# Optimization experiments

Measured on AMD Instinct MI355X. Metric: run time of the kernel, lower is better.

Reference implementation:

```python
import jax, jax.numpy as jnp
import numpy as np

N_USERS = 50000
N_ITEMS = 150000
N = N_USERS + N_ITEMS
N_EDGES = 1250000
D = 64
N_LAYERS = 3


def setup_inputs() -> dict:
    key = jax.random.key(0)
    ks = jax.random.split(key, 7)
    edge_src = jax.random.randint(ks[0], (N_EDGES,), 0, N, dtype=jnp.int32)
    edge_dst = jax.random.randint(ks[1], (N_EDGES,), 0, N, dtype=jnp.int32)
    edge_weight = jax.random.uniform(ks[2], (N_EDGES,), dtype=jnp.float32)
    user_emb = jax.random.normal(ks[3], (N_USERS, D), dtype=jnp.float32) * 0.1
    item_emb = jax.random.normal(ks[4], (N_ITEMS, D), dtype=jnp.float32) * 0.1
    # Ws[layer, which_linear] with which_linear in {0: W1 (on L@e), 1: W2 (on (L@e)*e), 2: W3 (on e)}
    Ws = jax.random.normal(ks[5], (N_LAYERS, 3, D, D), dtype=jnp.float32) * (1.0 / np.sqrt(D))
    bs = jnp.zeros((N_LAYERS, 3, D), dtype=jnp.float32)
    return {"edge_src": edge_src, "edge_dst": edge_dst, "edge_weight": edge_weight,
            "user_emb": user_emb, "item_emb": item_emb, "Ws": Ws, "bs": bs}


def _l2_normalize(x):
    # torch.nn.functional.normalize(p=2, dim=1, eps=1e-12)
    n = jnp.sqrt(jnp.sum(x * x, axis=1, keepdims=True))
    return x / jnp.maximum(n, 1e-12)


def reference(edge_src, edge_dst, edge_weight, user_emb, item_emb, Ws, bs):
    e = jnp.concatenate([user_emb, item_emb], axis=0)  # [N, D]
    all_embs = [e]
    for i in range(N_LAYERS):
        # SpMM: term1 = L @ e (COO scatter-add)
        term1 = jax.ops.segment_sum(edge_weight[:, None] * e[edge_src], edge_dst,
                                    num_segments=N)  # [N, D]
        term2 = term1 * e
        inter = (term1 @ Ws[i, 0] + bs[i, 0]
                 + term2 @ Ws[i, 1] + bs[i, 1]
                 + e @ Ws[i, 2] + bs[i, 2])
        inter = jax.nn.leaky_relu(inter, negative_slope=0.01)
        e = _l2_normalize(inter)  # dropout is identity in eval mode
        all_embs.append(e)
    all_embs = jnp.concatenate(all_embs, axis=1)  # [N, 4*D]
    return all_embs[:N_USERS], all_embs[N_USERS:]
```

## Files before the change

kernel.cpp:

```cpp
#include <hip/hip_runtime.h>
#include <hip/hip_bf16.h>

#define NU 50000
#define NI 150000
#define NN 200000
#define NE 1250000
#define DD 64
#define NLAYERS 3
#define SCAN_B 1024
#define NB ((NN + SCAN_B - 1) / SCAN_B)
#define BT_STRIDE 232

typedef __attribute__((ext_vector_type(8))) short bf16x8;
typedef __attribute__((ext_vector_type(4))) float f32x4;

static __device__ __forceinline__ unsigned short f2b(float x) {
  __hip_bfloat16 h = __float2bfloat16(x);
  return *reinterpret_cast<unsigned short*>(&h);
}

static __device__ __forceinline__ unsigned int pack2(float lo, float hi) {
  return (unsigned int)f2b(lo) | ((unsigned int)f2b(hi) << 16);
}

static __device__ __forceinline__ float blo(unsigned int u) { return __uint_as_float(u << 16); }
static __device__ __forceinline__ float bhi(unsigned int u) { return __uint_as_float(u & 0xffff0000u); }

static __device__ __forceinline__ bf16x8 mulbf8(bf16x8 a, bf16x8 b) {
  union { bf16x8 v; unsigned int u[4]; } A, B, R;
  A.v = a; B.v = b;
#pragma unroll
  for (int i = 0; i < 4; ++i) {
    R.u[i] = pack2(blo(A.u[i]) * blo(B.u[i]), bhi(A.u[i]) * bhi(B.u[i]));
  }
  return R.v;
}

__global__ __launch_bounds__(256) void k_setup(const float4* __restrict__ ue,
                                               const float4* __restrict__ ie,
                                               float4* __restrict__ out4,
                                               uint2* __restrict__ ebf2,
                                               const float* __restrict__ Ws,
                                               unsigned short* __restrict__ WtBf,
                                               int* __restrict__ cnt) {
  int gid = blockIdx.x * 256 + threadIdx.x;
  if (gid < NN * 16) {
    int row = gid >> 4, q = gid & 15;
    float4 v = (row < NU) ? ue[(size_t)row * 16 + q] : ie[(size_t)(row - NU) * 16 + q];
    out4[(size_t)row * 64 + q] = v;
    uint2 b; b.x = pack2(v.x, v.y); b.y = pack2(v.z, v.w);
    ebf2[(size_t)row * 16 + q] = b;
  }
  if (gid < NN) cnt[gid] = 0;
  if (gid < 3 * 64 * 192) {
    int j = gid % 192;
    int n = (gid / 192) & 63;
    int lyr = gid / (192 * 64);
    WtBf[gid] = f2b(Ws[((size_t)lyr * 3 + (j >> 6)) * 4096 + (size_t)(j & 63) * 64 + n]);
  }
}

__global__ __launch_bounds__(256) void k_hist(const int* __restrict__ dst, int* __restrict__ cnt) {
  int e = blockIdx.x * 256 + threadIdx.x;
  if (e < NE) atomicAdd(&cnt[dst[e]], 1);
}

__global__ __launch_bounds__(SCAN_B) void k_scan1(const int* __restrict__ cnt,
                                                  int* __restrict__ local,
                                                  int* __restrict__ btot) {
  __shared__ int sm[SCAN_B];
  int t = threadIdx.x;
  int i = blockIdx.x * SCAN_B + t;
  int v = (i < NN) ? cnt[i] : 0;
  sm[t] = v;
  __syncthreads();
  for (int off = 1; off < SCAN_B; off <<= 1) {
    int x = (t >= off) ? sm[t - off] : 0;
    __syncthreads();
    sm[t] += x;
    __syncthreads();
  }
  if (i < NN) local[i] = sm[t] - v;
  if (t == SCAN_B - 1) btot[blockIdx.x] = sm[t];
}

__global__ __launch_bounds__(256) void k_scan2(int* __restrict__ btot) {
  __shared__ int sm[256];
  int t = threadIdx.x;
  int v = (t < NB) ? btot[t] : 0;
  sm[t] = v;
  __syncthreads();
  for (int off = 1; off < 256; off <<= 1) {
    int x = (t >= off) ? sm[t - off] : 0;
    __syncthreads();
    sm[t] += x;
    __syncthreads();
  }
  if (t < NB) btot[t] = sm[t] - v;
}

__global__ __launch_bounds__(256) void k_finalize(const int* __restrict__ local,
                                                  const int* __restrict__ btot,
                                                  int* __restrict__ row_start,
                                                  int* __restrict__ cursor) {
  int i = blockIdx.x * 256 + threadIdx.x;
  if (i < NN) {
    int v = local[i] + btot[i / SCAN_B];
    row_start[i] = v;
    cursor[i] = v;
  }
  if (i == 0) row_start[NN] = NE;
}

__global__ __launch_bounds__(256) void k_fill(const int* __restrict__ src,
                                              const int* __restrict__ dst,
                                              const float* __restrict__ w,
                                              int* __restrict__ cursor,
                                              int2* __restrict__ csr_pack) {
  int e = blockIdx.x * 256 + threadIdx.x;
  if (e < NE) {
    int p = atomicAdd(&cursor[dst[e]], 1);
    int2 pk; pk.x = src[e]; pk.y = __float_as_int(w[e]);
    csr_pack[p] = pk;
  }
}

__global__ __launch_bounds__(256) void k_spmm(const int* __restrict__ row_start,
                                              const int2* __restrict__ csr_pack,
                                              const unsigned int* __restrict__ ebf,
                                              unsigned int* __restrict__ t1bf) {
  int gid = blockIdx.x * 256 + threadIdx.x;
  int row = gid >> 6;
  if (row >= NN) return;
  const int l = gid & 63;
  const int eidx = l >> 3;
  const int cb = l & 7;
  int s0 = row_start[row];
  int s1 = row_start[row + 1];
  int deg = s1 - s0;

  float a0 = 0.f, a1 = 0.f, a2 = 0.f, a3 = 0.f, a4 = 0.f, a5 = 0.f, a6 = 0.f, a7 = 0.f;

  if (deg > 0) {
    int j0 = s0 + eidx;
    bool e0 = j0 < s1;
    j0 = e0 ? j0 : s1 - 1;
    int2 p0 = csr_pack[j0];
    uint4 v0 = *reinterpret_cast<const uint4*>(ebf + (size_t)p0.x * 32 + cb * 4);
    float w0 = e0 ? __int_as_float(p0.y) : 0.f;
    if (deg > 8) {
      int j1 = s0 + 8 + eidx;
      bool e1 = j1 < s1;
      j1 = e1 ? j1 : s1 - 1;
      int2 p1 = csr_pack[j1];
      uint4 v1 = *reinterpret_cast<const uint4*>(ebf + (size_t)p1.x * 32 + cb * 4);
      float w1 = e1 ? __int_as_float(p1.y) : 0.f;
      a0 = fmaf(w0, blo(v0.x), a0); a1 = fmaf(w0, bhi(v0.x), a1);
      a2 = fmaf(w0, blo(v0.y), a2); a3 = fmaf(w0, bhi(v0.y), a3);
      a4 = fmaf(w0, blo(v0.z), a4); a5 = fmaf(w0, bhi(v0.z), a5);
      a6 = fmaf(w0, blo(v0.w), a6); a7 = fmaf(w0, bhi(v0.w), a7);
      a0 = fmaf(w1, blo(v1.x), a0); a1 = fmaf(w1, bhi(v1.x), a1);
      a2 = fmaf(w1, blo(v1.y), a2); a3 = fmaf(w1, bhi(v1.y), a3);
      a4 = fmaf(w1, blo(v1.z), a4); a5 = fmaf(w1, bhi(v1.z), a5);
      a6 = fmaf(w1, blo(v1.w), a6); a7 = fmaf(w1, bhi(v1.w), a7);
      for (int base = s0 + 16; base < s1; base += 8) {
        int j = base + eidx;
        bool ev = j < s1;
        j = ev ? j : s1 - 1;
        int2 p = csr_pack[j];
        uint4 v = *reinterpret_cast<const uint4*>(ebf + (size_t)p.x * 32 + cb * 4);
        float wt = ev ? __int_as_float(p.y) : 0.f;
        a0 = fmaf(wt, blo(v.x), a0); a1 = fmaf(wt, bhi(v.x), a1);
        a2 = fmaf(wt, blo(v.y), a2); a3 = fmaf(wt, bhi(v.y), a3);
        a4 = fmaf(wt, blo(v.z), a4); a5 = fmaf(wt, bhi(v.z), a5);
        a6 = fmaf(wt, blo(v.w), a6); a7 = fmaf(wt, bhi(v.w), a7);
      }
    } else {
      a0 = fmaf(w0, blo(v0.x), a0); a1 = fmaf(w0, bhi(v0.x), a1);
      a2 = fmaf(w0, blo(v0.y), a2); a3 = fmaf(w0, bhi(v0.y), a3);
      a4 = fmaf(w0, blo(v0.z), a4); a5 = fmaf(w0, bhi(v0.z), a5);
      a6 = fmaf(w0, blo(v0.w), a6); a7 = fmaf(w0, bhi(v0.w), a7);
    }
  }

  a0 += __shfl_xor(a0, 8, 64);  a0 += __shfl_xor(a0, 16, 64);  a0 += __shfl_xor(a0, 32, 64);
  a1 += __shfl_xor(a1, 8, 64);  a1 += __shfl_xor(a1, 16, 64);  a1 += __shfl_xor(a1, 32, 64);
  a2 += __shfl_xor(a2, 8, 64);  a2 += __shfl_xor(a2, 16, 64);  a2 += __shfl_xor(a2, 32, 64);
  a3 += __shfl_xor(a3, 8, 64);  a3 += __shfl_xor(a3, 16, 64);  a3 += __shfl_xor(a3, 32, 64);
  a4 += __shfl_xor(a4, 8, 64);  a4 += __shfl_xor(a4, 16, 64);  a4 += __shfl_xor(a4, 32, 64);
  a5 += __shfl_xor(a5, 8, 64);  a5 += __shfl_xor(a5, 16, 64);  a5 += __shfl_xor(a5, 32, 64);
  a6 += __shfl_xor(a6, 8, 64);  a6 += __shfl_xor(a6, 16, 64);  a6 += __shfl_xor(a6, 32, 64);
  a7 += __shfl_xor(a7, 8, 64);  a7 += __shfl_xor(a7, 16, 64);  a7 += __shfl_xor(a7, 32, 64);

  if (l < 8) {
    uint4 st;
    st.x = pack2(a0, a1); st.y = pack2(a2, a3); st.z = pack2(a4, a5); st.w = pack2(a6, a7);
    *reinterpret_cast<uint4*>(t1bf + (size_t)row * 32 + l * 4) = st;
  }
}

__global__ __launch_bounds__(512) void k_row_mfma(const unsigned int* __restrict__ t1bf,
                                                  const unsigned int* __restrict__ ebf,
                                                  const unsigned short* __restrict__ WtBf,
                                                  const float* __restrict__ bs,
                                                  float* __restrict__ out,
                                                  unsigned short* __restrict__ ebf_next,
                                                  int layer, int wbf) {
  __shared__ unsigned short Bt[64][BT_STRIDE];
  const int tid = threadIdx.x;
  {
    const uint4* __restrict__ src = reinterpret_cast<const uint4*>(WtBf + (size_t)layer * 64 * 192);
#pragma unroll
    for (int ch = tid; ch < 1536; ch += 512) {
      int rown = ch / 24, k = ch % 24;
      *reinterpret_cast<uint4*>(&Bt[rown][k * 8]) = src[ch];
    }
  }
  __syncthreads();

  const int l = tid & 63;
  const int wv = tid >> 6;
  const int g = l >> 4;
  const int li = l & 15;
  const int rowbase = blockIdx.x * 128 + wv * 16;
  if (rowbase >= NN) return;
  const int r = rowbase + li;

  const unsigned short* __restrict__ t1b = reinterpret_cast<const unsigned short*>(t1bf);
  const unsigned short* __restrict__ eb = reinterpret_cast<const unsigned short*>(ebf);
  bf16x8 A0 = *reinterpret_cast<const bf16x8*>(t1b + (size_t)r * 64 + 8 * g);
  bf16x8 A1 = *reinterpret_cast<const bf16x8*>(t1b + (size_t)r * 64 + 32 + 8 * g);
  bf16x8 E0 = *reinterpret_cast<const bf16x8*>(eb + (size_t)r * 64 + 8 * g);
  bf16x8 E1 = *reinterpret_cast<const bf16x8*>(eb + (size_t)r * 64 + 32 + 8 * g);
  bf16x8 T0 = mulbf8(A0, E0);
  bf16x8 T1 = mulbf8(A1, E1);

  const float* __restrict__ bsl = bs + (size_t)layer * 3 * 64;
  f32x4 acc[4];
#pragma unroll
  for (int f = 0; f < 4; ++f) {
    int n = f * 16 + li;
    float bv = bsl[n] + bsl[64 + n] + bsl[128 + n];
    acc[f] = (f32x4){bv, bv, bv, bv};
  }

  bf16x8 Afr[6] = {A0, A1, T0, T1, E0, E1};
#pragma unroll
  for (int s = 0; s < 6; ++s) {
#pragma unroll
    for (int f = 0; f < 4; ++f) {
      const bf16x8 Bf = *reinterpret_cast<const bf16x8*>(&Bt[f * 16 + li][s * 32 + 8 * g]);
      acc[f] = __builtin_amdgcn_mfma_f32_16x16x32_bf16(Afr[s], Bf, acc[f], 0, 0, 0);
    }
  }

  float p[4];
#pragma unroll
  for (int reg = 0; reg < 4; ++reg) {
    float ssum = 0.f;
#pragma unroll
    for (int f = 0; f < 4; ++f) {
      float x = acc[f][reg];
      x = (x >= 0.f) ? x : 0.01f * x;
      acc[f][reg] = x;
      ssum = fmaf(x, x, ssum);
    }
    p[reg] = ssum;
  }
#pragma unroll
  for (int off = 1; off < 16; off <<= 1) {
#pragma unroll
    for (int reg = 0; reg < 4; ++reg) p[reg] += __shfl_xor(p[reg], off, 64);
  }
  float inv[4];
#pragma unroll
  for (int reg = 0; reg < 4; ++reg) inv[reg] = 1.0f / fmaxf(sqrtf(p[reg]), 1e-12f);

  float* __restrict__ ob = out + (size_t)(layer + 1) * 64;
#pragma unroll
  for (int reg = 0; reg < 4; ++reg) {
#pragma unroll
    for (int f = 0; f < 4; ++f) {
      float val = acc[f][reg] * inv[reg];
      ob[(size_t)(rowbase + 4 * g + reg) * 256 + f * 16 + li] = val;
      if (wbf) ebf_next[(size_t)(rowbase + 4 * g + reg) * 64 + f * 16 + li] = f2b(val);
    }
  }
}

extern "C" void kernel_launch(void* const* d_in, const int* in_sizes, int n_in,
                              void* d_out, int out_size, void* d_ws, size_t ws_size,
                              hipStream_t stream) {
  const int* edge_src = (const int*)d_in[0];
  const int* edge_dst = (const int*)d_in[1];
  const float* edge_w = (const float*)d_in[2];
  const float* user_emb = (const float*)d_in[3];
  const float* item_emb = (const float*)d_in[4];
  const float* Ws = (const float*)d_in[5];
  const float* bs = (const float*)d_in[6];
  float* out = (float*)d_out;

  char* w = (char*)d_ws;
  unsigned int* ebfA = (unsigned int*)w; w += (size_t)NN * 32 * 4;
  unsigned int* ebfB = (unsigned int*)w; w += (size_t)NN * 32 * 4;
  unsigned int* t1bf = (unsigned int*)w; w += (size_t)NN * 32 * 4;
  int2* csr_pack = (int2*)w;      w += (size_t)NE * 8;
  unsigned short* WtBf = (unsigned short*)w; w += (size_t)3 * 64 * 192 * 2;
  int* cnt = (int*)w;             w += (size_t)NN * 4;
  int* local = (int*)w;           w += (size_t)NN * 4;
  int* row_start = (int*)w;       w += (size_t)(NN + 4) * 4;
  int* cursor = (int*)w;          w += (size_t)NN * 4;
  int* btot = (int*)w;            w += 256 * 4;

  k_setup<<<(NN * 16 + 255) / 256, 256, 0, stream>>>(
      (const float4*)user_emb, (const float4*)item_emb, (float4*)out, (uint2*)ebfA,
      Ws, WtBf, cnt);
  k_hist<<<(NE + 255) / 256, 256, 0, stream>>>(edge_dst, cnt);
  k_scan1<<<NB, SCAN_B, 0, stream>>>(cnt, local, btot);
  k_scan2<<<1, 256, 0, stream>>>(btot);
  k_finalize<<<(NN + 255) / 256, 256, 0, stream>>>(local, btot, row_start, cursor);
  k_fill<<<(NE + 255) / 256, 256, 0, stream>>>(edge_src, edge_dst, edge_w, cursor, csr_pack);

  k_spmm<<<(NN * 64 + 255) / 256, 256, 0, stream>>>(row_start, csr_pack, ebfA, t1bf);
  k_row_mfma<<<(NN + 127) / 128, 512, 0, stream>>>(t1bf, ebfA, WtBf, bs, out, (unsigned short*)ebfB, 0, 1);
  k_spmm<<<(NN * 64 + 255) / 256, 256, 0, stream>>>(row_start, csr_pack, ebfB, t1bf);
  k_row_mfma<<<(NN + 127) / 128, 512, 0, stream>>>(t1bf, ebfB, WtBf, bs, out, (unsigned short*)ebfA, 1, 1);
  k_spmm<<<(NN * 64 + 255) / 256, 256, 0, stream>>>(row_start, csr_pack, ebfA, t1bf);
  k_row_mfma<<<(NN + 127) / 128, 512, 0, stream>>>(t1bf, ebfA, WtBf, bs, out, (unsigned short*)ebfB, 2, 0);
}
```

Baseline: 412.6 us.

## Fuse SpMM with per-row MFMA transform into one layer kernel; merge setup with histogram

Each layer now runs as one kernel. Sixteen waves each gather one row's neighbours into shared memory, then four waves run the MFMA transform on those 16 rows, each wave handling a 16-column slice, with the L2 norm reduced across waves through shared memory. This drops the t1 round trip through global memory and one launch per layer. The cost is that every 1024-thread block loads the full 24 KB weight tile for only 16 rows, and 12 of the 16 waves sit idle during the MFMA phase. Separately, the setup and histogram kernels are merged into one launch, with a small kernel added in front to zero the counters.

```diff
diff --git a/kernel.cpp b/kernel.cpp
--- a/kernel.cpp
+++ b/kernel.cpp
@@ -10,6 +10,8 @@
 #define SCAN_B 1024
 #define NB ((NN + SCAN_B - 1) / SCAN_B)
 #define BT_STRIDE 232
+#define SETUP_BLKS 12500
+#define HIST_BLKS ((NE + 255) / 256)
 
 typedef __attribute__((ext_vector_type(8))) short bf16x8;
 typedef __attribute__((ext_vector_type(4))) float f32x4;
@@ -36,33 +38,37 @@
   return R.v;
 }
 
-__global__ __launch_bounds__(256) void k_setup(const float4* __restrict__ ue,
-                                               const float4* __restrict__ ie,
-                                               float4* __restrict__ out4,
-                                               uint2* __restrict__ ebf2,
-                                               const float* __restrict__ Ws,
-                                               unsigned short* __restrict__ WtBf,
-                                               int* __restrict__ cnt) {
-  int gid = blockIdx.x * 256 + threadIdx.x;
-  if (gid < NN * 16) {
+__global__ __launch_bounds__(256) void k_zero(int* __restrict__ p) {
+  int i = blockIdx.x * 256 + threadIdx.x;
+  if (i < NN) p[i] = 0;
+}
+
+__global__ __launch_bounds__(256) void k_setup_hist(const float4* __restrict__ ue,
+                                                    const float4* __restrict__ ie,
+                                                    float4* __restrict__ out4,
+                                                    uint2* __restrict__ ebf2,
+                                                    const float* __restrict__ Ws,
+                                                    unsigned short* __restrict__ WtBf,
+                                                    const int* __restrict__ dst,
+                                                    int* __restrict__ cnt) {
+  int bid = blockIdx.x;
+  if (bid < SETUP_BLKS) {
+    int gid = bid * 256 + threadIdx.x;
     int row = gid >> 4, q = gid & 15;
     float4 v = (row < NU) ? ue[(size_t)row * 16 + q] : ie[(size_t)(row - NU) * 16 + q];
     out4[(size_t)row * 64 + q] = v;
     uint2 b; b.x = pack2(v.x, v.y); b.y = pack2(v.z, v.w);
     ebf2[(size_t)row * 16 + q] = b;
-  }
-  if (gid < NN) cnt[gid] = 0;
-  if (gid < 3 * 64 * 192) {
-    int j = gid % 192;
-    int n = (gid / 192) & 63;
-    int lyr = gid / (192 * 64);
-    WtBf[gid] = f2b(Ws[((size_t)lyr * 3 + (j >> 6)) * 4096 + (size_t)(j & 63) * 64 + n]);
-  }
-}
-
-__global__ __launch_bounds__(256) void k_hist(const int* __restrict__ dst, int* __restrict__ cnt) {
-  int e = blockIdx.x * 256 + threadIdx.x;
-  if (e < NE) atomicAdd(&cnt[dst[e]], 1);
+    if (gid < 3 * 64 * 192) {
+      int j = gid % 192;
+      int n = (gid / 192) & 63;
+      int lyr = gid / (192 * 64);
+      WtBf[gid] = f2b(Ws[((size_t)lyr * 3 + (j >> 6)) * 4096 + (size_t)(j & 63) * 64 + n]);
+    }
+  } else {
+    int e = (bid - SETUP_BLKS) * 256 + threadIdx.x;
+    if (e < NE) atomicAdd(&cnt[dst[e]], 1);
+  }
 }
 
 __global__ __launch_bounds__(SCAN_B) void k_scan1(const int* __restrict__ cnt,
@@ -125,165 +131,155 @@
   }
 }
 
-__global__ __launch_bounds__(256) void k_spmm(const int* __restrict__ row_start,
-                                              const int2* __restrict__ csr_pack,
-                                              const unsigned int* __restrict__ ebf,
-                                              unsigned int* __restrict__ t1bf) {
-  int gid = blockIdx.x * 256 + threadIdx.x;
-  int row = gid >> 6;
-  if (row >= NN) return;
-  const int l = gid & 63;
-  const int eidx = l >> 3;
-  const int cb = l & 7;
-  int s0 = row_start[row];
-  int s1 = row_start[row + 1];
-  int deg = s1 - s0;
-
-  float a0 = 0.f, a1 = 0.f, a2 = 0.f, a3 = 0.f, a4 = 0.f, a5 = 0.f, a6 = 0.f, a7 = 0.f;
-
-  if (deg > 0) {
-    int j0 = s0 + eidx;
-    bool e0 = j0 < s1;
-    j0 = e0 ? j0 : s1 - 1;
-    int2 p0 = csr_pack[j0];
-    uint4 v0 = *reinterpret_cast<const uint4*>(ebf + (size_t)p0.x * 32 + cb * 4);
-    float w0 = e0 ? __int_as_float(p0.y) : 0.f;
-    if (deg > 8) {
-      int j1 = s0 + 8 + eidx;
-      bool e1 = j1 < s1;
-      j1 = e1 ? j1 : s1 - 1;
-      int2 p1 = csr_pack[j1];
-      uint4 v1 = *reinterpret_cast<const uint4*>(ebf + (size_t)p1.x * 32 + cb * 4);
-      float w1 = e1 ? __int_as_float(p1.y) : 0.f;
-      a0 = fmaf(w0, blo(v0.x), a0); a1 = fmaf(w0, bhi(v0.x), a1);
-      a2 = fmaf(w0, blo(v0.y), a2); a3 = fmaf(w0, bhi(v0.y), a3);
-      a4 = fmaf(w0, blo(v0.z), a4); a5 = fmaf(w0, bhi(v0.z), a5);
-      a6 = fmaf(w0, blo(v0.w), a6); a7 = fmaf(w0, bhi(v0.w), a7);
-      a0 = fmaf(w1, blo(v1.x), a0); a1 = fmaf(w1, bhi(v1.x), a1);
-      a2 = fmaf(w1, blo(v1.y), a2); a3 = fmaf(w1, bhi(v1.y), a3);
-      a4 = fmaf(w1, blo(v1.z), a4); a5 = fmaf(w1, bhi(v1.z), a5);
-      a6 = fmaf(w1, blo(v1.w), a6); a7 = fmaf(w1, bhi(v1.w), a7);
-      for (int base = s0 + 16; base < s1; base += 8) {
-        int j = base + eidx;
-        bool ev = j < s1;
-        j = ev ? j : s1 - 1;
-        int2 p = csr_pack[j];
-        uint4 v = *reinterpret_cast<const uint4*>(ebf + (size_t)p.x * 32 + cb * 4);
-        float wt = ev ? __int_as_float(p.y) : 0.f;
-        a0 = fmaf(wt, blo(v.x), a0); a1 = fmaf(wt, bhi(v.x), a1);
-        a2 = fmaf(wt, blo(v.y), a2); a3 = fmaf(wt, bhi(v.y), a3);
-        a4 = fmaf(wt, blo(v.z), a4); a5 = fmaf(wt, bhi(v.z), a5);
-        a6 = fmaf(wt, blo(v.w), a6); a7 = fmaf(wt, bhi(v.w), a7);
-      }
-    } else {
-      a0 = fmaf(w0, blo(v0.x), a0); a1 = fmaf(w0, bhi(v0.x), a1);
-      a2 = fmaf(w0, blo(v0.y), a2); a3 = fmaf(w0, bhi(v0.y), a3);
-      a4 = fmaf(w0, blo(v0.z), a4); a5 = fmaf(w0, bhi(v0.z), a5);
-      a6 = fmaf(w0, blo(v0.w), a6); a7 = fmaf(w0, bhi(v0.w), a7);
-    }
-  }
-
-  a0 += __shfl_xor(a0, 8, 64);  a0 += __shfl_xor(a0, 16, 64);  a0 += __shfl_xor(a0, 32, 64);
-  a1 += __shfl_xor(a1, 8, 64);  a1 += __shfl_xor(a1, 16, 64);  a1 += __shfl_xor(a1, 32, 64);
-  a2 += __shfl_xor(a2, 8, 64);  a2 += __shfl_xor(a2, 16, 64);  a2 += __shfl_xor(a2, 32, 64);
-  a3 += __shfl_xor(a3, 8, 64);  a3 += __shfl_xor(a3, 16, 64);  a3 += __shfl_xor(a3, 32, 64);
-  a4 += __shfl_xor(a4, 8, 64);  a4 += __shfl_xor(a4, 16, 64);  a4 += __shfl_xor(a4, 32, 64);
-  a5 += __shfl_xor(a5, 8, 64);  a5 += __shfl_xor(a5, 16, 64);  a5 += __shfl_xor(a5, 32, 64);
-  a6 += __shfl_xor(a6, 8, 64);  a6 += __shfl_xor(a6, 16, 64);  a6 += __shfl_xor(a6, 32, 64);
-  a7 += __shfl_xor(a7, 8, 64);  a7 += __shfl_xor(a7, 16, 64);  a7 += __shfl_xor(a7, 32, 64);
-
-  if (l < 8) {
-    uint4 st;
-    st.x = pack2(a0, a1); st.y = pack2(a2, a3); st.z = pack2(a4, a5); st.w = pack2(a6, a7);
-    *reinterpret_cast<uint4*>(t1bf + (size_t)row * 32 + l * 4) = st;
-  }
-}
-
-__global__ __launch_bounds__(512) void k_row_mfma(const unsigned int* __restrict__ t1bf,
-                                                  const unsigned int* __restrict__ ebf,
-                                                  const unsigned short* __restrict__ WtBf,
-                                                  const float* __restrict__ bs,
-                                                  float* __restrict__ out,
-                                                  unsigned short* __restrict__ ebf_next,
-                                                  int layer, int wbf) {
+__global__ __launch_bounds__(1024, 8) void k_layer(const int* __restrict__ row_start,
+                                                   const int2* __restrict__ csr_pack,
+                                                   const unsigned int* __restrict__ ebf,
+                                                   const unsigned short* __restrict__ WtBf,
+                                                   const float* __restrict__ bs,
+                                                   float* __restrict__ out,
+                                                   unsigned short* __restrict__ ebf_next,
+                                                   int layer, int wbf) {
   __shared__ unsigned short Bt[64][BT_STRIDE];
+  __shared__ unsigned short t1s[16][72];
+  __shared__ float rsum[4][16];
+
   const int tid = threadIdx.x;
+  const int wv = tid >> 6;
+  const int l = tid & 63;
+
   {
     const uint4* __restrict__ src = reinterpret_cast<const uint4*>(WtBf + (size_t)layer * 64 * 192);
-#pragma unroll
-    for (int ch = tid; ch < 1536; ch += 512) {
+    for (int ch = tid; ch < 1536; ch += 1024) {
       int rown = ch / 24, k = ch % 24;
       *reinterpret_cast<uint4*>(&Bt[rown][k * 8]) = src[ch];
     }
   }
+
+  {
+    const int row = blockIdx.x * 16 + wv;
+    const int eidx = l >> 3;
+    const int cb = l & 7;
+    int s0 = row_start[row];
+    int s1 = row_start[row + 1];
+    int deg = s1 - s0;
+
+    float a0 = 0.f, a1 = 0.f, a2 = 0.f, a3 = 0.f, a4 = 0.f, a5 = 0.f, a6 = 0.f, a7 = 0.f;
+
+    if (deg > 0) {
+      int j0 = s0 + eidx;
+      bool e0 = j0 < s1;
+      j0 = e0 ? j0 : s1 - 1;
+      int2 p0 = csr_pack[j0];
+      uint4 v0 = *reinterpret_cast<const uint4*>(ebf + (size_t)p0.x * 32 + cb * 4);
+      float w0 = e0 ? __int_as_float(p0.y) : 0.f;
+      if (deg > 8) {
+        int j1 = s0 + 8 + eidx;
+        bool e1 = j1 < s1;
+        j1 = e1 ? j1 : s1 - 1;
+        int2 p1 = csr_pack[j1];
+        uint4 v1 = *reinterpret_cast<const uint4*>(ebf + (size_t)p1.x * 32 + cb * 4);
+        float w1 = e1 ? __int_as_float(p1.y) : 0.f;
+        a0 = fmaf(w0, blo(v0.x), a0); a1 = fmaf(w0, bhi(v0.x), a1);
+        a2 = fmaf(w0, blo(v0.y), a2); a3 = fmaf(w0, bhi(v0.y), a3);
+        a4 = fmaf(w0, blo(v0.z), a4); a5 = fmaf(w0, bhi(v0.z), a5);
+        a6 = fmaf(w0, blo(v0.w), a6); a7 = fmaf(w0, bhi(v0.w), a7);
+        a0 = fmaf(w1, blo(v1.x), a0); a1 = fmaf(w1, bhi(v1.x), a1);
+        a2 = fmaf(w1, blo(v1.y), a2); a3 = fmaf(w1, bhi(v1.y), a3);
+        a4 = fmaf(w1, blo(v1.z), a4); a5 = fmaf(w1, bhi(v1.z), a5);
+        a6 = fmaf(w1, blo(v1.w), a6); a7 = fmaf(w1, bhi(v1.w), a7);
+        for (int base = s0 + 16; base < s1; base += 8) {
+          int j = base + eidx;
+          bool ev = j < s1;
+          j = ev ? j : s1 - 1;
+          int2 p = csr_pack[j];
+          uint4 v = *reinterpret_cast<const uint4*>(ebf + (size_t)p.x * 32 + cb * 4);
+          float wt = ev ? __int_as_float(p.y) : 0.f;
+          a0 = fmaf(wt, blo(v.x), a0); a1 = fmaf(wt, bhi(v.x), a1);
+          a2 = fmaf(wt, blo(v.y), a2); a3 = fmaf(wt, bhi(v.y), a3);
+          a4 = fmaf(wt, blo(v.z), a4); a5 = fmaf(wt, bhi(v.z), a5);
+          a6 = fmaf(wt, blo(v.w), a6); a7 = fmaf(wt, bhi(v.w), a7);
+        }
+      } else {
+        a0 = fmaf(w0, blo(v0.x), a0); a1 = fmaf(w0, bhi(v0.x), a1);
+        a2 = fmaf(w0, blo(v0.y), a2); a3 = fmaf(w0, bhi(v0.y), a3);
+        a4 = fmaf(w0, blo(v0.z), a4); a5 = fmaf(w0, bhi(v0.z), a5);
+        a6 = fmaf(w0, blo(v0.w), a6); a7 = fmaf(w0, bhi(v0.w), a7);
+      }
+    }
+
+    a0 += __shfl_xor(a0, 8, 64);  a0 += __shfl_xor(a0, 16, 64);  a0 += __shfl_xor(a0, 32, 64);
+    a1 += __shfl_xor(a1, 8, 64);  a1 += __shfl_xor(a1, 16, 64);  a1 += __shfl_xor(a1, 32, 64);
+    a2 += __shfl_xor(a2, 8, 64);  a2 += __shfl_xor(a2, 16, 64);  a2 += __shfl_xor(a2, 32, 64);
+    a3 += __shfl_xor(a3, 8, 64);  a3 += __shfl_xor(a3, 16, 64);  a3 += __shfl_xor(a3, 32, 64);
+    a4 += __shfl_xor(a4, 8, 64);  a4 += __shfl_xor(a4, 16, 64);  a4 += __shfl_xor(a4, 32, 64);
+    a5 += __shfl_xor(a5, 8, 64);  a5 += __shfl_xor(a5, 16, 64);  a5 += __shfl_xor(a5, 32, 64);
+    a6 += __shfl_xor(a6, 8, 64);  a6 += __shfl_xor(a6, 16, 64);  a6 += __shfl_xor(a6, 32, 64);
+    a7 += __shfl_xor(a7, 8, 64);  a7 += __shfl_xor(a7, 16, 64);  a7 += __shfl_xor(a7, 32, 64);
+
+    if (l < 8) {
+      uint4 st;
+      st.x = pack2(a0, a1); st.y = pack2(a2, a3); st.z = pack2(a4, a5); st.w = pack2(a6, a7);
+      *reinterpret_cast<uint4*>(&t1s[wv][l * 8]) = st;
+    }
+  }
   __syncthreads();
 
-  const int l = tid & 63;
-  const int wv = tid >> 6;
   const int g = l >> 4;
   const int li = l & 15;
-  const int rowbase = blockIdx.x * 128 + wv * 16;
-  if (rowbase >= NN) return;
-  const int r = rowbase + li;
-
-  const unsigned short* __restrict__ t1b = reinterpret_cast<const unsigned short*>(t1bf);
-  const unsigned short* __restrict__ eb = reinterpret_cast<const unsigned short*>(ebf);
-  bf16x8 A0 = *reinterpret_cast<const bf16x8*>(t1b + (size_t)r * 64 + 8 * g);
-  bf16x8 A1 = *reinterpret_cast<const bf16x8*>(t1b + (size_t)r * 64 + 32 + 8 * g);
-  bf16x8 E0 = *reinterpret_cast<const bf16x8*>(eb + (size_t)r * 64 + 8 * g);
-  bf16x8 E1 = *reinterpret_cast<const bf16x8*>(eb + (size_t)r * 64 + 32 + 8 * g);
-  bf16x8 T0 = mulbf8(A0, E0);
-  bf16x8 T1 = mulbf8(A1, E1);
-
-  const float* __restrict__ bsl = bs + (size_t)layer * 3 * 64;
-  f32x4 acc[4];
-#pragma unroll
-  for (int f = 0; f < 4; ++f) {
-    int n = f * 16 + li;
+  f32x4 acc = (f32x4){0.f, 0.f, 0.f, 0.f};
+  if (wv < 4) {
+    const int r = blockIdx.x * 16 + li;
+    bf16x8 A0 = *reinterpret_cast<const bf16x8*>(&t1s[li][8 * g]);
+    bf16x8 A1 = *reinterpret_cast<const bf16x8*>(&t1s[li][32 + 8 * g]);
+    const unsigned short* __restrict__ eb = reinterpret_cast<const unsigned short*>(ebf);
+    bf16x8 E0 = *reinterpret_cast<const bf16x8*>(eb + (size_t)r * 64 + 8 * g);
+    bf16x8 E1 = *reinterpret_cast<const bf16x8*>(eb + (size_t)r * 64 + 32 + 8 * g);
+    bf16x8 T0 = mulbf8(A0, E0);
+    bf16x8 T1 = mulbf8(A1, E1);
+
+    const float* __restrict__ bsl = bs + (size_t)layer * 3 * 64;
+    int n = wv * 16 + li;
     float bv = bsl[n] + bsl[64 + n] + bsl[128 + n];
-    acc[f] = (f32x4){bv, bv, bv, bv};
-  }
-
-  bf16x8 Afr[6] = {A0, A1, T0, T1, E0, E1};
-#pragma unroll
-  for (int s = 0; s < 6; ++s) {
-#pragma unroll
-    for (int f = 0; f < 4; ++f) {
-      const bf16x8 Bf = *reinterpret_cast<const bf16x8*>(&Bt[f * 16 + li][s * 32 + 8 * g]);
-      acc[f] = __builtin_amdgcn_mfma_f32_16x16x32_bf16(Afr[s], Bf, acc[f], 0, 0, 0);
-    }
-  }
-
-  float p[4];
-#pragma unroll
-  for (int reg = 0; reg < 4; ++reg) {
-    float ssum = 0.f;
-#pragma unroll
-    for (int f = 0; f < 4; ++f) {
-      float x = acc[f][reg];
+    acc = (f32x4){bv, bv, bv, bv};
+
+    bf16x8 Afr[6] = {A0, A1, T0, T1, E0, E1};
+#pragma unroll
+    for (int s = 0; s < 6; ++s) {
+      const bf16x8 Bf = *reinterpret_cast<const bf16x8*>(&Bt[wv * 16 + li][s * 32 + 8 * g]);
+      acc = __builtin_amdgcn_mfma_f32_16x16x32_bf16(Afr[s], Bf, acc, 0, 0, 0);
+    }
+
+    float p[4];
+#pragma unroll
+    for (int reg = 0; reg < 4; ++reg) {
+      float x = acc[reg];
       x = (x >= 0.f) ? x : 0.01f * x;
-      acc[f][reg] = x;
-      ssum = fmaf(x, x, ssum);
-    }
-    p[reg] = ssum;
-  }
-#pragma unroll
-  for (int off = 1; off < 16; off <<= 1) {
-#pragma unroll
-    for (int reg = 0; reg < 4; ++reg) p[reg] += __shfl_xor(p[reg], off, 64);
-  }
-  float inv[4];
-#pragma unroll
-  for (int reg = 0; reg < 4; ++reg) inv[reg] = 1.0f / fmaxf(sqrtf(p[reg]), 1e-12f);
-
-  float* __restrict__ ob = out + (size_t)(layer + 1) * 64;
-#pragma unroll
-  for (int reg = 0; reg < 4; ++reg) {
-#pragma unroll
-    for (int f = 0; f < 4; ++f) {
-      float val = acc[f][reg] * inv[reg];
-      ob[(size_t)(rowbase + 4 * g + reg) * 256 + f * 16 + li] = val;
-      if (wbf) ebf_next[(size_t)(rowbase + 4 * g + reg) * 64 + f * 16 + li] = f2b(val);
+      acc[reg] = x;
+      p[reg] = x * x;
+    }
+#pragma unroll
+    for (int off = 1; off < 16; off <<= 1) {
+#pragma unroll
+      for (int reg = 0; reg < 4; ++reg) p[reg] += __shfl_xor(p[reg], off, 64);
+    }
+    if (li == 0) {
+#pragma unroll
+      for (int reg = 0; reg < 4; ++reg) rsum[wv][4 * g + reg] = p[reg];
+    }
+  }
+  __syncthreads();
+
+  if (wv < 4) {
+    const int rowbase = blockIdx.x * 16;
+    float* __restrict__ ob = out + (size_t)(layer + 1) * 64;
+#pragma unroll
+    for (int reg = 0; reg < 4; ++reg) {
+      int rr = 4 * g + reg;
+      float tot = rsum[0][rr] + rsum[1][rr] + rsum[2][rr] + rsum[3][rr];
+      float inv = 1.0f / fmaxf(sqrtf(tot), 1e-12f);
+      float val = acc[reg] * inv;
+      ob[(size_t)(rowbase + rr) * 256 + wv * 16 + li] = val;
+      if (wbf) ebf_next[(size_t)(rowbase + rr) * 64 + wv * 16 + li] = f2b(val);
     }
   }
 }
@@ -303,7 +299,6 @@
   char* w = (char*)d_ws;
   unsigned int* ebfA = (unsigned int*)w; w += (size_t)NN * 32 * 4;
   unsigned int* ebfB = (unsigned int*)w; w += (size_t)NN * 32 * 4;
-  unsigned int* t1bf = (unsigned int*)w; w += (size_t)NN * 32 * 4;
   int2* csr_pack = (int2*)w;      w += (size_t)NE * 8;
   unsigned short* WtBf = (unsigned short*)w; w += (size_t)3 * 64 * 192 * 2;
   int* cnt = (int*)w;             w += (size_t)NN * 4;
@@ -312,19 +307,19 @@
   int* cursor = (int*)w;          w += (size_t)NN * 4;
   int* btot = (int*)w;            w += 256 * 4;
 
-  k_setup<<<(NN * 16 + 255) / 256, 256, 0, stream>>>(
+  k_zero<<<(NN + 255) / 256, 256, 0, stream>>>(cnt);
+  k_setup_hist<<<SETUP_BLKS + HIST_BLKS, 256, 0, stream>>>(
       (const float4*)user_emb, (const float4*)item_emb, (float4*)out, (uint2*)ebfA,
-      Ws, WtBf, cnt);
-  k_hist<<<(NE + 255) / 256, 256, 0, stream>>>(edge_dst, cnt);
+      Ws, WtBf, edge_dst, cnt);
   k_scan1<<<NB, SCAN_B, 0, stream>>>(cnt, local, btot);
   k_scan2<<<1, 256, 0, stream>>>(btot);
   k_finalize<<<(NN + 255) / 256, 256, 0, stream>>>(local, btot, row_start, cursor);
   k_fill<<<(NE + 255) / 256, 256, 0, stream>>>(edge_src, edge_dst, edge_w, cursor, csr_pack);
 
-  k_spmm<<<(NN * 64 + 255) / 256, 256, 0, stream>>>(row_start, csr_pack, ebfA, t1bf);
-  k_row_mfma<<<(NN + 127) / 128, 512, 0, stream>>>(t1bf, ebfA, WtBf, bs, out, (unsigned short*)ebfB, 0, 1);
-  k_spmm<<<(NN * 64 + 255) / 256, 256, 0, stream>>>(row_start, csr_pack, ebfB, t1bf);
-  k_row_mfma<<<(NN + 127) / 128, 512, 0, stream>>>(t1bf, ebfB, WtBf, bs, out, (unsigned short*)ebfA, 1, 1);
-  k_spmm<<<(NN * 64 + 255) / 256, 256, 0, stream>>>(row_start, csr_pack, ebfA, t1bf);
-  k_row_mfma<<<(NN + 127) / 128, 512, 0, stream>>>(t1bf, ebfA, WtBf, bs, out, (unsigned short*)ebfB, 2, 0);
-}
+  k_layer<<<NN / 16, 1024, 0, stream>>>(row_start, csr_pack, ebfA, WtBf, bs, out,
+                                        (unsigned short*)ebfB, 0, 1);
+  k_layer<<<NN / 16, 1024, 0, stream>>>(row_start, csr_pack, ebfB, WtBf, bs, out,
+                                        (unsigned short*)ebfA, 1, 1);
+  k_layer<<<NN / 16, 1024, 0, stream>>>(row_start, csr_pack, ebfA, WtBf, bs, out,
+                                        (unsigned short*)ebfB, 2, 0);
+}
```

After: 521.6 us. 26.4% more time.
